# Performance work log

Measured on AMD Instinct MI355X. Metric: run time of the kernel, lower is better.

The kernel has to match this reference:

```python
import jax, jax.numpy as jnp
import numpy as np
from jax import lax

B, N, C = 4, 3072, 512
SAMPLE_RATIO = 0.25
CLUSTER_NUM = int(np.ceil(N * SAMPLE_RATIO))  # 768, static (mask=None, no 'r')
K = 5  # self.k, since k <= cluster_num


def setup_inputs() -> dict:
    key = jax.random.key(0)
    k1, = jax.random.split(key, 1)
    x = jax.random.normal(k1, (B, N, C), dtype=jnp.float32)
    # idx_token starts as identity mapping per batch (standard TCFormer init)
    idx_token = jnp.tile(jnp.arange(N, dtype=jnp.int32)[None, :], (B, 1))
    agg_weight = jnp.ones((B, N, 1), dtype=jnp.float32)
    return {"x": x, "idx_token": idx_token, "agg_weight": agg_weight}


def _cluster_dpc_knn(x):
    # runs under no_grad in torch -> stop_gradient here
    xs = lax.stop_gradient(x).astype(jnp.float32)
    sq = jnp.sum(xs * xs, axis=-1)  # [B,N]
    d2 = sq[:, :, None] + sq[:, None, :] - 2.0 * jnp.einsum('bnc,bmc->bnm', xs, xs)
    dist = jnp.sqrt(jnp.maximum(d2, 0.0)) / jnp.sqrt(jnp.float32(C))  # cdist / C**0.5
    # k nearest (smallest) distances
    neg_nearest, _ = lax.top_k(-dist, K)
    dist_nearest = -neg_nearest  # [B,N,K]
    density = jnp.exp(-jnp.mean(dist_nearest ** 2, axis=-1))
    density = density + jax.random.uniform(jax.random.key(42), density.shape, dtype=density.dtype) * 1e-6
    mask = (density[:, None, :] > density[:, :, None]).astype(x.dtype)  # [B,N,N]
    dist_max = jnp.max(dist.reshape(B, -1), axis=-1)[:, None, None]
    dist_min = jnp.min(dist * mask + dist_max * (1.0 - mask), axis=-1)  # [B,N]
    score = dist_min * density
    _, index_down = lax.top_k(score, CLUSTER_NUM)  # [B,cluster]
    # gather rows of dist at cluster centers, assign each token to nearest center
    dmat = jnp.take_along_axis(dist, index_down[:, :, None], axis=1)  # [B,cluster,N]
    idx_cluster = jnp.argmin(dmat, axis=1).astype(jnp.int32)  # [B,N]
    # force centers to map to their own cluster id
    idx_cluster = idx_cluster.at[jnp.arange(B)[:, None], index_down].set(
        jnp.broadcast_to(jnp.arange(CLUSTER_NUM, dtype=jnp.int32)[None, :], (B, CLUSTER_NUM)))
    return idx_cluster


def reference(x, idx_token, agg_weight):
    idx_cluster = _cluster_dpc_knn(x)
    # merge_tokens
    token_weight = jnp.ones((B, N, 1), dtype=x.dtype)
    idx = idx_cluster + jnp.arange(B, dtype=jnp.int32)[:, None] * CLUSTER_NUM  # [B,N]
    idx_flat = idx.reshape(-1)
    all_weight = jax.ops.segment_sum(token_weight.reshape(-1), idx_flat,
                                     num_segments=B * CLUSTER_NUM) + 1e-6  # [B*cluster]
    norm_weight = token_weight / all_weight[idx_flat].reshape(B, N, 1)  # [B,N,1]
    x_merged = jax.ops.segment_sum((x * norm_weight).reshape(B * N, C), idx_flat,
                                   num_segments=B * CLUSTER_NUM).reshape(B, CLUSTER_NUM, C)
    idx_token_new = jnp.take_along_axis(idx_cluster, idx_token, axis=1)  # [B,N]
    weight_t = jnp.take_along_axis(norm_weight, idx_token[:, :, None], axis=1)  # [B,N,1]
    agg_weight_new = agg_weight * weight_t
    return x_merged, agg_weight_new, idx_token_new, idx_cluster
```

## Files before the change

### kernel.cpp

```cpp
#include <hip/hip_runtime.h>
#include <math.h>
#include <float.h>

constexpr int B  = 4;
constexpr int N  = 3072;
constexpr int C  = 512;
constexpr int CL = 768;

typedef unsigned short u16;
typedef __attribute__((ext_vector_type(8))) short s16x8;
typedef __attribute__((ext_vector_type(4))) float f32x4;

__device__ __forceinline__ unsigned rotl32(unsigned v, int d) { return (v << d) | (v >> (32 - d)); }

__device__ inline void threefry2x32(unsigned k0, unsigned k1, unsigned c0, unsigned c1,
                                    unsigned& o0, unsigned& o1) {
  unsigned ks0 = k0, ks1 = k1, ks2 = 0x1BD11BDAu ^ k0 ^ k1;
  unsigned x0 = c0 + ks0, x1 = c1 + ks1;
#define TF_RND(r) { x0 += x1; x1 = rotl32(x1, (r)); x1 ^= x0; }
  TF_RND(13) TF_RND(15) TF_RND(26) TF_RND(6)  x0 += ks1; x1 += ks2 + 1u;
  TF_RND(17) TF_RND(29) TF_RND(16) TF_RND(24) x0 += ks2; x1 += ks0 + 2u;
  TF_RND(13) TF_RND(15) TF_RND(26) TF_RND(6)  x0 += ks0; x1 += ks1 + 3u;
  TF_RND(17) TF_RND(29) TF_RND(16) TF_RND(24) x0 += ks1; x1 += ks2 + 4u;
  TF_RND(13) TF_RND(15) TF_RND(26) TF_RND(6)  x0 += ks2; x1 += ks0 + 5u;
#undef TF_RND
  o0 = x0; o1 = x1;
}

__device__ inline float jax_uniform_bn(int f) {
  constexpr int HALF = (B * N) / 2;
  unsigned o0, o1, bits;
  if (f < HALF) { threefry2x32(0u, 42u, (unsigned)f, (unsigned)(f + HALF), o0, o1); bits = o0; }
  else          { threefry2x32(0u, 42u, (unsigned)(f - HALF), (unsigned)f, o0, o1); bits = o1; }
  return __uint_as_float((bits >> 9) | 0x3f800000u) - 1.0f;
}

__device__ __forceinline__ u16 bf16rn(float f) {
  unsigned u = __float_as_uint(f);
  unsigned r = u + 0x7FFFu + ((u >> 16) & 1u);
  return (u16)(r >> 16);
}
__device__ __forceinline__ float bf16tof(u16 h) {
  return __uint_as_float(((unsigned)h) << 16);
}

__global__ __launch_bounds__(64) void k_prep(const float* __restrict__ x, float* __restrict__ sq,
                                             u16* __restrict__ xhi, u16* __restrict__ xlo,
                                             int* __restrict__ counts,
                                             unsigned long long* __restrict__ packed,
                                             float* __restrict__ distmax) {
  int row = blockIdx.x;
  int lane = threadIdx.x;
  const float* xr = x + (size_t)row * C;
  u16* hr = xhi + (size_t)row * C;
  u16* lr = xlo + (size_t)row * C;
  float s = 0.f;
  for (int c = lane * 4; c < C; c += 256) {
    float4 v = *(const float4*)(xr + c);
    s += v.x * v.x + v.y * v.y + v.z * v.z + v.w * v.w;
    u16 h0 = bf16rn(v.x), h1 = bf16rn(v.y), h2 = bf16rn(v.z), h3 = bf16rn(v.w);
    u16 l0 = bf16rn(v.x - bf16tof(h0));
    u16 l1 = bf16rn(v.y - bf16tof(h1));
    u16 l2 = bf16rn(v.z - bf16tof(h2));
    u16 l3 = bf16rn(v.w - bf16tof(h3));
    uint2 hp, lp;
    hp.x = (unsigned)h0 | ((unsigned)h1 << 16); hp.y = (unsigned)h2 | ((unsigned)h3 << 16);
    lp.x = (unsigned)l0 | ((unsigned)l1 << 16); lp.y = (unsigned)l2 | ((unsigned)l3 << 16);
    *(uint2*)(hr + c) = hp;
    *(uint2*)(lr + c) = lp;
  }
  for (int o = 32; o > 0; o >>= 1) s += __shfl_down(s, o, 64);
  if (lane == 0) {
    sq[row] = s;
    packed[row] = ~0ull;
    if (row < B * CL) counts[row] = 0;
    if (row < B) distmax[row] = 0.f;
  }
}

__device__ __forceinline__ void ins5b(float t[5], float v) {
  float c = v;
  float n;
  n = fminf(t[0], c); c = fmaxf(t[0], c); t[0] = n;
  n = fminf(t[1], c); c = fmaxf(t[1], c); t[1] = n;
  n = fminf(t[2], c); c = fmaxf(t[2], c); t[2] = n;
  n = fminf(t[3], c); c = fmaxf(t[3], c); t[3] = n;
  t[4] = fminf(t[4], c);
}

constexpr int NT3 = N / 128;
constexpr int NTILE3 = NT3 * (NT3 + 1) / 2;

__global__ __launch_bounds__(256, 2) void k_distm(const u16* __restrict__ xhi, const u16* __restrict__ xlo,
                                                  const float* __restrict__ sq,
                                                  float* __restrict__ distbuf,
                                                  float* __restrict__ part5, int b0) {
  __shared__ __align__(16) char smem[65536];
  u16* smem_u16 = (u16*)smem;

  int bl = blockIdx.y, b = b0 + bl;

  int bx = blockIdx.x;
  constexpr int NX = 8, QX = NTILE3 / NX, RX = NTILE3 % NX;
  int xcd = bx % NX, sub = bx / NX;
  int idx = (xcd < RX ? xcd * (QX + 1) : RX * (QX + 1) + (xcd - RX) * QX) + sub;

  int ti = 0, rem = idx;
  while (rem >= NT3 - ti) { rem -= NT3 - ti; ++ti; }
  int tj = ti + rem;
  int i0 = ti * 128, j0 = tj * 128;
  bool do_mirror = (ti != tj);

  const float* sqb = sq + (size_t)b * N;
  float* dist = distbuf + (size_t)bl * N * N;

  int tid = threadIdx.x;
  int lane = tid & 63, w = tid >> 6;
  int wr = (w >> 1) * 64, wc = (w & 1) * 64;
  int l15 = lane & 15, l4 = lane >> 4;
  int csw = (lane >> 1) & 3;

  const u16* hil = (w & 1) ? xlo : xhi;
  int rbase0 = (w < 2) ? i0 : j0;
  const u16* gsrc = hil + ((size_t)b * N + rbase0 + (lane >> 2)) * C
                        + ((lane & 3) ^ ((lane >> 3) & 3)) * 8;

  f32x4 acc[4][4];
#pragma unroll
  for (int rt = 0; rt < 4; ++rt)
#pragma unroll
    for (int ct = 0; ct < 4; ++ct)
#pragma unroll
      for (int e = 0; e < 4; ++e) acc[rt][ct][e] = 0.f;

  {
    u16* lb = smem_u16 + w * 4096;
#pragma unroll
    for (int q = 0; q < 8; ++q)
      __builtin_amdgcn_global_load_lds(
          (const __attribute__((address_space(1))) void*)(gsrc + q * 16 * C),
          (__attribute__((address_space(3))) void*)(lb + q * 512), 16, 0, 0);
  }
  __syncthreads();

#define KSTEP(CUR, STG, KNXT, DO_STAGE)                                              \
  {                                                                                  \
    if (DO_STAGE) {                                                                  \
      u16* lb = smem_u16 + (STG) * 16384 + w * 4096;                                 \
      const u16* gs = gsrc + (KNXT);                                                 \
      _Pragma("unroll")                                                              \
      for (int q = 0; q < 8; ++q)                                                    \
        __builtin_amdgcn_global_load_lds(                                            \
            (const __attribute__((address_space(1))) void*)(gs + q * 16 * C),        \
            (__attribute__((address_space(3))) void*)(lb + q * 512), 16, 0, 0);      \
    }                                                                                \
    const u16* sb = smem_u16 + (CUR) * 16384;                                        \
    s16x8 ah[4], al[4];                                                              \
    _Pragma("unroll")                                                                \
    for (int rt = 0; rt < 4; ++rt) {                                                 \
      int ro = (wr + rt * 16 + l15) * 32 + (l4 ^ csw) * 8;                           \
      ah[rt] = *(const s16x8*)(sb + ro);                                             \
      al[rt] = *(const s16x8*)(sb + 4096 + ro);                                      \
    }                                                                                \
    _Pragma("unroll")                                                                \
    for (int ct = 0; ct < 4; ++ct) {                                                 \
      int co = (wc + ct * 16 + l15) * 32 + (l4 ^ csw) * 8;                           \
      s16x8 bh = *(const s16x8*)(sb + 8192 + co);                                    \
      s16x8 bl = *(const s16x8*)(sb + 12288 + co);                                   \
      _Pragma("unroll")                                                              \
      for (int rt = 0; rt < 4; ++rt) {                                               \
        acc[rt][ct] = __builtin_amdgcn_mfma_f32_16x16x32_bf16(ah[rt], bh, acc[rt][ct], 0, 0, 0); \
        acc[rt][ct] = __builtin_amdgcn_mfma_f32_16x16x32_bf16(ah[rt], bl, acc[rt][ct], 0, 0, 0); \
        acc[rt][ct] = __builtin_amdgcn_mfma_f32_16x16x32_bf16(al[rt], bh, acc[rt][ct], 0, 0, 0); \
      }                                                                              \
    }                                                                                \
    __syncthreads();                                                                 \
  }

  for (int ks = 0; ks < 16; ks += 2) {
    KSTEP(0, 1, (ks + 1) * 32, true)
    KSTEP(1, 0, (ks + 2) * 32, (ks + 2 < 16))
  }
#undef KSTEP

  const float SQC = 22.627416997969522f;
  float sqi[4][4], sqj[4];
#pragma unroll
  for (int rt = 0; rt < 4; ++rt)
#pragma unroll
    for (int r = 0; r < 4; ++r) sqi[rt][r] = sqb[i0 + wr + rt * 16 + l4 * 4 + r];
#pragma unroll
  for (int ct = 0; ct < 4; ++ct) sqj[ct] = sqb[j0 + wc + ct * 16 + l15];

#pragma unroll
  for (int rt = 0; rt < 4; ++rt)
#pragma unroll
    for (int ct = 0; ct < 4; ++ct)
#pragma unroll
      for (int r = 0; r < 4; ++r) {
        float d2 = fmaxf(sqi[rt][r] + sqj[ct] - 2.0f * acc[rt][ct][r], 0.0f);
        acc[rt][ct][r] = sqrtf(d2) / SQC;
      }

  constexpr int TSTR = 77;
  float* sT = (float*)smem + w * (32 * TSTR);

  float t5A[5] = {FLT_MAX, FLT_MAX, FLT_MAX, FLT_MAX, FLT_MAX};
  float mxA = 0.f;

#pragma unroll
  for (int p = 0; p < 2; ++p) {
#pragma unroll
    for (int cth = 0; cth < 2; ++cth) {
      int ct = p * 2 + cth;
      int cl = cth * 16 + l15;
#pragma unroll
      for (int rt = 0; rt < 4; ++rt)
#pragma unroll
        for (int r = 0; r < 4; ++r)
          sT[cl * TSTR + rt * 16 + l4 * 4 + r] = acc[rt][ct][r];
    }
    {
      int g4 = lane & 7, rbase = lane >> 3;
#pragma unroll
      for (int it = 0; it < 8; ++it) {
        int rl = it * 8 + rbase;
        float4 v = make_float4(sT[(4 * g4 + 0) * TSTR + rl],
                               sT[(4 * g4 + 1) * TSTR + rl],
                               sT[(4 * g4 + 2) * TSTR + rl],
                               sT[(4 * g4 + 3) * TSTR + rl]);
        *(float4*)(dist + (size_t)(i0 + wr + rl) * N + j0 + wc + p * 32 + 4 * g4) = v;
      }
    }
    if (do_mirror) {
      int cg = lane >> 4, rq = lane & 15;
#pragma unroll
      for (int cc = 0; cc < 8; ++cc) {
        int c = cc * 4 + cg;
        float4 v;
        v.x = sT[c * TSTR + rq * 4 + 0];
        v.y = sT[c * TSTR + rq * 4 + 1];
        v.z = sT[c * TSTR + rq * 4 + 2];
        v.w = sT[c * TSTR + rq * 4 + 3];
        *(float4*)(dist + (size_t)(j0 + wc + p * 32 + c) * N + i0 + wr + rq * 4) = v;
      }
    }
    for (int c = 0; c < 32; ++c) {
      float v = sT[c * TSTR + lane];
      mxA = fmaxf(mxA, v);
      ins5b(t5A, v);
    }
    if (do_mirror) {
      int cl = lane & 31, half = lane >> 5;
      float t5B[5] = {FLT_MAX, FLT_MAX, FLT_MAX, FLT_MAX, FLT_MAX};
      float mxB = 0.f;
      for (int k = 0; k < 32; ++k) {
        float v = sT[cl * TSTR + half * 32 + k];
        mxB = fmaxf(mxB, v);
        ins5b(t5B, v);
      }
      mxB = fmaxf(mxB, __shfl_xor(mxB, 32, 64));
      float o0 = __shfl_xor(t5B[0], 32, 64);
      float o1 = __shfl_xor(t5B[1], 32, 64);
      float o2 = __shfl_xor(t5B[2], 32, 64);
      float o3 = __shfl_xor(t5B[3], 32, 64);
      float o4 = __shfl_xor(t5B[4], 32, 64);
      ins5b(t5B, o0); ins5b(t5B, o1); ins5b(t5B, o2); ins5b(t5B, o3); ins5b(t5B, o4);
      if (half == 0) {
        int rowB = j0 + wc + p * 32 + cl;
        int slotB = ti * 2 + (wr >> 6);
        float* dst = part5 + (((size_t)bl * 48 + slotB) * 6) * N + rowB;
        dst[0] = t5B[0]; dst[(size_t)N] = t5B[1]; dst[2 * (size_t)N] = t5B[2];
        dst[3 * (size_t)N] = t5B[3]; dst[4 * (size_t)N] = t5B[4]; dst[5 * (size_t)N] = mxB;
      }
    }
  }
  {
    int rowA = i0 + wr + lane;
    int slotA = tj * 2 + (wc >> 6);
    float* dst = part5 + (((size_t)bl * 48 + slotA) * 6) * N + rowA;
    dst[0] = t5A[0]; dst[(size_t)N] = t5A[1]; dst[2 * (size_t)N] = t5A[2];
    dst[3 * (size_t)N] = t5A[3]; dst[4 * (size_t)N] = t5A[4]; dst[5 * (size_t)N] = mxA;
  }
}

__global__ __launch_bounds__(256) void k_dens(const float* __restrict__ part5,
                                              float* __restrict__ density,
                                              float* __restrict__ distmax, int b0) {
  int g = blockIdx.x * 256 + threadIdx.x;
  int bl = g / N, r = g % N;
  int b = b0 + bl;
  const float* base = part5 + (size_t)bl * 48 * 6 * N + r;
  float t5[5] = {FLT_MAX, FLT_MAX, FLT_MAX, FLT_MAX, FLT_MAX};
  float mx = 0.f;
  for (int s = 0; s < 48; ++s) {
    const float* sp = base + (size_t)s * 6 * N;
    ins5b(t5, sp[0]);
    ins5b(t5, sp[(size_t)N]);
    ins5b(t5, sp[2 * (size_t)N]);
    ins5b(t5, sp[3 * (size_t)N]);
    ins5b(t5, sp[4 * (size_t)N]);
    mx = fmaxf(mx, sp[5 * (size_t)N]);
  }
  float sum = t5[0] * t5[0] + t5[1] * t5[1] + t5[2] * t5[2] + t5[3] * t5[3] + t5[4] * t5[4];
  density[b * N + r] = expf(-(sum / 5.0f)) + jax_uniform_bn(b * N + r) * 1e-6f;
#pragma unroll
  for (int m = 1; m < 64; m <<= 1) mx = fmaxf(mx, __shfl_xor(mx, m, 64));
  if ((threadIdx.x & 63) == 0) atomicMax((int*)(distmax + b), __float_as_int(mx));
}

__global__ __launch_bounds__(256) void k_maskmin(const float* __restrict__ distbuf,
                                                 const float* __restrict__ density,
                                                 const float* __restrict__ distmax,
                                                 float* __restrict__ score, int b0) {
  __shared__ float sd[N];
  int tid = threadIdx.x;
  int wv = tid >> 6, lane = tid & 63;
  int i = blockIdx.x * 4 + wv;
  int bl = blockIdx.y, b = b0 + bl;
  const float* db = density + (size_t)b * N;
  for (int j = tid * 4; j < N; j += 1024) *(float4*)(sd + j) = *(const float4*)(db + j);
  __syncthreads();
  float di = sd[i];
  float dmax = distmax[b];
  const float* row = distbuf + ((size_t)bl * N + i) * N;
  float mn = dmax;
#pragma unroll
  for (int it = 0; it < N / 256; ++it) {
    int j = it * 256 + lane * 4;
    float4 v = *(const float4*)(row + j);
    float4 d = *(const float4*)(sd + j);
    mn = fminf(mn, (d.x > di) ? v.x : dmax);
    mn = fminf(mn, (d.y > di) ? v.y : dmax);
    mn = fminf(mn, (d.z > di) ? v.z : dmax);
    mn = fminf(mn, (d.w > di) ? v.w : dmax);
  }
#pragma unroll
  for (int m = 1; m < 64; m <<= 1) mn = fminf(mn, __shfl_xor(mn, m, 64));
  if (lane == 0) score[b * N + i] = mn * di;
}

__global__ __launch_bounds__(256) void k_rank(const float* __restrict__ score,
                                              int* __restrict__ index_down,
                                              int* __restrict__ rank, int b0) {
  __shared__ float ssc[N];
  int tid = threadIdx.x;
  int wv = tid >> 6, lane = tid & 63;
  int i = blockIdx.x * 4 + wv;
  int b = b0 + blockIdx.y;
  const float* sb = score + (size_t)b * N;
  for (int j = tid * 4; j < N; j += 1024) *(float4*)(ssc + j) = *(const float4*)(sb + j);
  __syncthreads();
  float si = ssc[i];
  int cnt = 0;
#pragma unroll
  for (int it = 0; it < N / 256; ++it) {
    int j = it * 256 + lane * 4;
    float4 v = *(const float4*)(ssc + j);
    cnt += (v.x > si) || (v.x == si && (j + 0) < i);
    cnt += (v.y > si) || (v.y == si && (j + 1) < i);
    cnt += (v.z > si) || (v.z == si && (j + 2) < i);
    cnt += (v.w > si) || (v.w == si && (j + 3) < i);
  }
#pragma unroll
  for (int m = 1; m < 64; m <<= 1) cnt += __shfl_xor(cnt, m, 64);
  if (lane == 0) {
    rank[b * N + i] = (cnt < CL) ? cnt : -1;
    if (cnt < CL) index_down[b * CL + cnt] = i;
  }
}

__global__ __launch_bounds__(256) void k_assign_part(const float* __restrict__ distbuf,
                                                     const int* __restrict__ index_down,
                                                     unsigned long long* __restrict__ packed, int b0) {
  constexpr int RCH = CL / 8;
  __shared__ int sid[RCH];
  int bl = blockIdx.z, b = b0 + bl;
  int r0 = blockIdx.y * RCH;
  int tid = threadIdx.x;
  for (int r = tid; r < RCH; r += 256) sid[r] = index_down[b * CL + r0 + r];
  __syncthreads();
  int j = blockIdx.x * 256 + tid;
  const float* base = distbuf + (size_t)bl * N * N;
  float best = FLT_MAX; int bestr = 0;
#pragma unroll 8
  for (int r = 0; r < RCH; ++r) {
    float d = base[(size_t)sid[r] * N + j];
    if (d < best) { best = d; bestr = r0 + r; }
  }
  unsigned long long key = ((unsigned long long)__float_as_uint(best) << 32) | (unsigned)bestr;
  atomicMin(&packed[b * N + j], key);
}

__global__ void k_assign_fin2(const unsigned long long* __restrict__ packed,
                              const int* __restrict__ rank,
                              int* __restrict__ idx_cluster, int* __restrict__ counts) {
  int g = blockIdx.x * 256 + threadIdx.x;
  int b = g / N;
  int r = rank[g];
  int cl = (r >= 0) ? r : (int)(unsigned)(packed[g] & 0xffffffffull);
  idx_cluster[g] = cl;
  atomicAdd(&counts[b * CL + cl], 1);
}

__global__ __launch_bounds__(1024) void k_scan(const int* __restrict__ counts,
                                               int* __restrict__ offsets, int* __restrict__ cursor) {
  constexpr int T = B * CL;
  __shared__ int sm[T];
  int tid = threadIdx.x;
  for (int p = tid; p < T; p += 1024) sm[p] = counts[p];
  __syncthreads();
  for (int off = 1; off < T; off <<= 1) {
    int v[3]; int n = 0;
    for (int p = tid; p < T; p += 1024) { v[n++] = (p >= off) ? sm[p - off] : 0; }
    __syncthreads();
    n = 0;
    for (int p = tid; p < T; p += 1024) { sm[p] += v[n++]; }
    __syncthreads();
  }
  for (int p = tid; p < T; p += 1024) {
    int e = sm[p] - counts[p];
    offsets[p] = e; cursor[p] = e;
  }
}

__global__ void k_fill(const int* __restrict__ idx_cluster, int* __restrict__ cursor,
                       int* __restrict__ members) {
  int g = blockIdx.x * 256 + threadIdx.x;
  int b = g / N, i = g % N;
  int seg = b * CL + idx_cluster[g];
  int pos = atomicAdd(&cursor[seg], 1);
  members[pos] = i;
}

__global__ __launch_bounds__(128) void k_gather(const float* __restrict__ x, const int* __restrict__ members,
                                                const int* __restrict__ offsets, const int* __restrict__ counts,
                                                float* __restrict__ out0) {
  int seg = blockIdx.x;
  int b = seg / CL;
  int cnt = counts[seg], off = offsets[seg];
  float nw = 1.0f / ((float)cnt + 1e-6f);
  int c = threadIdx.x * 4;
  const float* xb = x + (size_t)b * N * C;
  float4 acc = make_float4(0.f, 0.f, 0.f, 0.f);
  for (int m = 0; m < cnt; ++m) {
    int tok = members[off + m];
    float4 v = *(const float4*)(xb + (size_t)tok * C + c);
    acc.x += v.x * nw; acc.y += v.y * nw; acc.z += v.z * nw; acc.w += v.w * nw;
  }
  *(float4*)(out0 + (size_t)seg * C + c) = acc;
}

__global__ void k_final(const float* __restrict__ agg_weight, const int* __restrict__ idx_token,
                        const int* __restrict__ idx_cluster, const int* __restrict__ counts,
                        float* __restrict__ out1, float* __restrict__ out2, float* __restrict__ out3) {
  int g = blockIdx.x * 256 + threadIdx.x;
  int b = g / N;
  int it = idx_token[g];
  int clt = idx_cluster[b * N + it];
  float nwt = 1.0f / ((float)counts[b * CL + clt] + 1e-6f);
  out1[g] = agg_weight[g] * nwt;
  out2[g] = (float)clt;
  out3[g] = (float)idx_cluster[g];
}

extern "C" void kernel_launch(void* const* d_in, const int* in_sizes, int n_in,
                              void* d_out, int out_size, void* d_ws, size_t ws_size,
                              hipStream_t stream) {
  const float* x          = (const float*)d_in[0];
  const int*   idx_token  = (const int*)d_in[1];
  const float* agg_weight = (const float*)d_in[2];

  float* out0 = (float*)d_out;
  float* out1 = out0 + (size_t)B * CL * C;
  float* out2 = out1 + (size_t)B * N;
  float* out3 = out2 + (size_t)B * N;

  char* w = (char*)d_ws;
  auto carve = [&](size_t bytes) { char* p = w; w += (bytes + 255) & ~(size_t)255; return p; };
  float*    sq         = (float*)carve((size_t)B * N * 4);
  float*    density    = (float*)carve((size_t)B * N * 4);
  float*    score      = (float*)carve((size_t)B * N * 4);
  float*    distmax    = (float*)carve((size_t)B * 4);
  int*      index_down = (int*)carve((size_t)B * CL * 4);
  int*      rank       = (int*)carve((size_t)B * N * 4);
  int*      idx_clus   = (int*)carve((size_t)B * N * 4);
  int*      counts     = (int*)carve((size_t)B * CL * 4);
  int*      offsets    = (int*)carve((size_t)B * CL * 4);
  int*      cursor     = (int*)carve((size_t)B * CL * 4);
  int*      members    = (int*)carve((size_t)B * N * 4);
  unsigned long long* packed = (unsigned long long*)carve((size_t)B * N * 8);
  u16*      xhi        = (u16*)carve((size_t)B * N * C * 2);
  u16*      xlo        = (u16*)carve((size_t)B * N * C * 2);
  float*    part5      = (float*)carve((size_t)B * 48 * 6 * N * 4);
  size_t used = (size_t)(w - (char*)d_ws);
  size_t per  = (size_t)N * N * 4;
  int nb_max = (ws_size > used) ? (int)((ws_size - used) / per) : 0;
  if (nb_max < 1) nb_max = 1;
  if (nb_max > B) nb_max = B;
  float* distbuf = (float*)w;

  k_prep<<<B * N, 64, 0, stream>>>(x, sq, xhi, xlo, counts, packed, distmax);

  for (int b0 = 0; b0 < B; b0 += nb_max) {
    int nb = (B - b0 < nb_max) ? (B - b0) : nb_max;
    k_distm<<<dim3(NTILE3, nb), 256, 0, stream>>>(xhi, xlo, sq, distbuf, part5, b0);
    k_dens<<<(nb * N) / 256, 256, 0, stream>>>(part5, density, distmax, b0);
    k_maskmin<<<dim3(N / 4, nb), 256, 0, stream>>>(distbuf, density, distmax, score, b0);
    k_rank<<<dim3(N / 4, nb), 256, 0, stream>>>(score, index_down, rank, b0);
    k_assign_part<<<dim3(N / 256, 8, nb), 256, 0, stream>>>(distbuf, index_down, packed, b0);
  }

  k_assign_fin2<<<(B * N) / 256, 256, 0, stream>>>(packed, rank, idx_clus, counts);
  k_scan<<<1, 1024, 0, stream>>>(counts, offsets, cursor);
  k_fill<<<(B * N) / 256, 256, 0, stream>>>(idx_clus, cursor, members);
  k_gather<<<B * CL, 128, 0, stream>>>(x, members, offsets, counts, out0);
  k_final<<<(B * N) / 256, 256, 0, stream>>>(agg_weight, idx_token, idx_clus, counts, out1, out2, out3);
}
```

Baseline: 294.2 us.

## Overlap GEMM LDS staging with partial vmcnt waits; batch four rows per wave

In the distance GEMM, the full __syncthreads after each k-step is replaced by raw s_barrier plus s_waitcnt vmcnt(8). This lets the next stage's global-to-LDS loads stay in flight while the current tile is consumed. The maskmin and rank kernels now process four rows per wave instead of one. That cuts the grid by four and reuses each LDS density/score load across four rows. The hand-placed waitcnt and barriers depend on exact counting of outstanding loads, and any miscount would be a correctness risk.

Result: no change. 293.3 us (-0.3%).

```diff
diff --git a/kernel.cpp b/kernel.cpp
--- a/kernel.cpp
+++ b/kernel.cpp
@@ -141,7 +141,6 @@
           (const __attribute__((address_space(1))) void*)(gsrc + q * 16 * C),
           (__attribute__((address_space(3))) void*)(lb + q * 512), 16, 0, 0);
   }
-  __syncthreads();
 
 #define KSTEP(CUR, STG, KNXT, DO_STAGE)                                              \
   {                                                                                  \
@@ -153,7 +152,12 @@
         __builtin_amdgcn_global_load_lds(                                            \
             (const __attribute__((address_space(1))) void*)(gs + q * 16 * C),        \
             (__attribute__((address_space(3))) void*)(lb + q * 512), 16, 0, 0);      \
+      asm volatile("s_waitcnt vmcnt(8)" ::: "memory");                               \
+    } else {                                                                         \
+      asm volatile("s_waitcnt vmcnt(0)" ::: "memory");                               \
     }                                                                                \
+    __builtin_amdgcn_s_barrier();                                                    \
+    asm volatile("" ::: "memory");                                                   \
     const u16* sb = smem_u16 + (CUR) * 16384;                                        \
     s16x8 ah[4], al[4];                                                              \
     _Pragma("unroll")                                                                \
@@ -174,7 +178,9 @@
         acc[rt][ct] = __builtin_amdgcn_mfma_f32_16x16x32_bf16(al[rt], bh, acc[rt][ct], 0, 0, 0); \
       }                                                                              \
     }                                                                                \
-    __syncthreads();                                                                 \
+    asm volatile("" ::: "memory");                                                   \
+    __builtin_amdgcn_s_barrier();                                                    \
+    asm volatile("" ::: "memory");                                                   \
   }
 
   for (int ks = 0; ks < 16; ks += 2) {
@@ -316,28 +322,53 @@
   __shared__ float sd[N];
   int tid = threadIdx.x;
   int wv = tid >> 6, lane = tid & 63;
-  int i = blockIdx.x * 4 + wv;
   int bl = blockIdx.y, b = b0 + bl;
   const float* db = density + (size_t)b * N;
   for (int j = tid * 4; j < N; j += 1024) *(float4*)(sd + j) = *(const float4*)(db + j);
   __syncthreads();
-  float di = sd[i];
+  int i0r = blockIdx.x * 16 + wv * 4;
   float dmax = distmax[b];
-  const float* row = distbuf + ((size_t)bl * N + i) * N;
-  float mn = dmax;
-#pragma unroll
+  const float* row0 = distbuf + ((size_t)bl * N + i0r) * N;
+  float di0 = sd[i0r], di1 = sd[i0r + 1], di2 = sd[i0r + 2], di3 = sd[i0r + 3];
+  float mn0 = dmax, mn1 = dmax, mn2 = dmax, mn3 = dmax;
+#pragma unroll 2
   for (int it = 0; it < N / 256; ++it) {
     int j = it * 256 + lane * 4;
-    float4 v = *(const float4*)(row + j);
-    float4 d = *(const float4*)(sd + j);
-    mn = fminf(mn, (d.x > di) ? v.x : dmax);
-    mn = fminf(mn, (d.y > di) ? v.y : dmax);
-    mn = fminf(mn, (d.z > di) ? v.z : dmax);
-    mn = fminf(mn, (d.w > di) ? v.w : dmax);
-  }
-#pragma unroll
-  for (int m = 1; m < 64; m <<= 1) mn = fminf(mn, __shfl_xor(mn, m, 64));
-  if (lane == 0) score[b * N + i] = mn * di;
+    float4 d  = *(const float4*)(sd + j);
+    float4 v0 = *(const float4*)(row0 + j);
+    float4 v1 = *(const float4*)(row0 + (size_t)N + j);
+    float4 v2 = *(const float4*)(row0 + 2 * (size_t)N + j);
+    float4 v3 = *(const float4*)(row0 + 3 * (size_t)N + j);
+    mn0 = fminf(mn0, (d.x > di0) ? v0.x : dmax);
+    mn0 = fminf(mn0, (d.y > di0) ? v0.y : dmax);
+    mn0 = fminf(mn0, (d.z > di0) ? v0.z : dmax);
+    mn0 = fminf(mn0, (d.w > di0) ? v0.w : dmax);
+    mn1 = fminf(mn1, (d.x > di1) ? v1.x : dmax);
+    mn1 = fminf(mn1, (d.y > di1) ? v1.y : dmax);
+    mn1 = fminf(mn1, (d.z > di1) ? v1.z : dmax);
+    mn1 = fminf(mn1, (d.w > di1) ? v1.w : dmax);
+    mn2 = fminf(mn2, (d.x > di2) ? v2.x : dmax);
+    mn2 = fminf(mn2, (d.y > di2) ? v2.y : dmax);
+    mn2 = fminf(mn2, (d.z > di2) ? v2.z : dmax);
+    mn2 = fminf(mn2, (d.w > di2) ? v2.w : dmax);
+    mn3 = fminf(mn3, (d.x > di3) ? v3.x : dmax);
+    mn3 = fminf(mn3, (d.y > di3) ? v3.y : dmax);
+    mn3 = fminf(mn3, (d.z > di3) ? v3.z : dmax);
+    mn3 = fminf(mn3, (d.w > di3) ? v3.w : dmax);
+  }
+#pragma unroll
+  for (int m = 1; m < 64; m <<= 1) {
+    mn0 = fminf(mn0, __shfl_xor(mn0, m, 64));
+    mn1 = fminf(mn1, __shfl_xor(mn1, m, 64));
+    mn2 = fminf(mn2, __shfl_xor(mn2, m, 64));
+    mn3 = fminf(mn3, __shfl_xor(mn3, m, 64));
+  }
+  if (lane == 0) {
+    score[b * N + i0r]     = mn0 * di0;
+    score[b * N + i0r + 1] = mn1 * di1;
+    score[b * N + i0r + 2] = mn2 * di2;
+    score[b * N + i0r + 3] = mn3 * di3;
+  }
 }
 
 __global__ __launch_bounds__(256) void k_rank(const float* __restrict__ score,
@@ -346,27 +377,50 @@
   __shared__ float ssc[N];
   int tid = threadIdx.x;
   int wv = tid >> 6, lane = tid & 63;
-  int i = blockIdx.x * 4 + wv;
   int b = b0 + blockIdx.y;
   const float* sb = score + (size_t)b * N;
   for (int j = tid * 4; j < N; j += 1024) *(float4*)(ssc + j) = *(const float4*)(sb + j);
   __syncthreads();
-  float si = ssc[i];
-  int cnt = 0;
-#pragma unroll
+  int i0r = blockIdx.x * 16 + wv * 4;
+  float s0 = ssc[i0r], s1 = ssc[i0r + 1], s2 = ssc[i0r + 2], s3 = ssc[i0r + 3];
+  int c0 = 0, c1 = 0, c2 = 0, c3 = 0;
+#pragma unroll 2
   for (int it = 0; it < N / 256; ++it) {
     int j = it * 256 + lane * 4;
     float4 v = *(const float4*)(ssc + j);
-    cnt += (v.x > si) || (v.x == si && (j + 0) < i);
-    cnt += (v.y > si) || (v.y == si && (j + 1) < i);
-    cnt += (v.z > si) || (v.z == si && (j + 2) < i);
-    cnt += (v.w > si) || (v.w == si && (j + 3) < i);
-  }
-#pragma unroll
-  for (int m = 1; m < 64; m <<= 1) cnt += __shfl_xor(cnt, m, 64);
+    c0 += (v.x > s0) || (v.x == s0 && (j + 0) < i0r);
+    c0 += (v.y > s0) || (v.y == s0 && (j + 1) < i0r);
+    c0 += (v.z > s0) || (v.z == s0 && (j + 2) < i0r);
+    c0 += (v.w > s0) || (v.w == s0 && (j + 3) < i0r);
+    c1 += (v.x > s1) || (v.x == s1 && (j + 0) < i0r + 1);
+    c1 += (v.y > s1) || (v.y == s1 && (j + 1) < i0r + 1);
+    c1 += (v.z > s1) || (v.z == s1 && (j + 2) < i0r + 1);
+    c1 += (v.w > s1) || (v.w == s1 && (j + 3) < i0r + 1);
+    c2 += (v.x > s2) || (v.x == s2 && (j + 0) < i0r + 2);
+    c2 += (v.y > s2) || (v.y == s2 && (j + 1) < i0r + 2);
+    c2 += (v.z > s2) || (v.z == s2 && (j + 2) < i0r + 2);
+    c2 += (v.w > s2) || (v.w == s2 && (j + 3) < i0r + 2);
+    c3 += (v.x > s3) || (v.x == s3 && (j + 0) < i0r + 3);
+    c3 += (v.y > s3) || (v.y == s3 && (j + 1) < i0r + 3);
+    c3 += (v.z > s3) || (v.z == s3 && (j + 2) < i0r + 3);
+    c3 += (v.w > s3) || (v.w == s3 && (j + 3) < i0r + 3);
+  }
+#pragma unroll
+  for (int m = 1; m < 64; m <<= 1) {
+    c0 += __shfl_xor(c0, m, 64);
+    c1 += __shfl_xor(c1, m, 64);
+    c2 += __shfl_xor(c2, m, 64);
+    c3 += __shfl_xor(c3, m, 64);
+  }
   if (lane == 0) {
-    rank[b * N + i] = (cnt < CL) ? cnt : -1;
-    if (cnt < CL) index_down[b * CL + cnt] = i;
+    rank[b * N + i0r]     = (c0 < CL) ? c0 : -1;
+    rank[b * N + i0r + 1] = (c1 < CL) ? c1 : -1;
+    rank[b * N + i0r + 2] = (c2 < CL) ? c2 : -1;
+    rank[b * N + i0r + 3] = (c3 < CL) ? c3 : -1;
+    if (c0 < CL) index_down[b * CL + c0] = i0r;
+    if (c1 < CL) index_down[b * CL + c1] = i0r + 1;
+    if (c2 < CL) index_down[b * CL + c2] = i0r + 2;
+    if (c3 < CL) index_down[b * CL + c3] = i0r + 3;
   }
 }
 
@@ -506,8 +560,8 @@
     int nb = (B - b0 < nb_max) ? (B - b0) : nb_max;
     k_distm<<<dim3(NTILE3, nb), 256, 0, stream>>>(xhi, xlo, sq, distbuf, part5, b0);
     k_dens<<<(nb * N) / 256, 256, 0, stream>>>(part5, density, distmax, b0);
-    k_maskmin<<<dim3(N / 4, nb), 256, 0, stream>>>(distbuf, density, distmax, score, b0);
-    k_rank<<<dim3(N / 4, nb), 256, 0, stream>>>(score, index_down, rank, b0);
+    k_maskmin<<<dim3(N / 16, nb), 256, 0, stream>>>(distbuf, density, distmax, score, b0);
+    k_rank<<<dim3(N / 16, nb), 256, 0, stream>>>(score, index_down, rank, b0);
     k_assign_part<<<dim3(N / 256, 8, nb), 256, 0, stream>>>(distbuf, index_down, packed, b0);
   }
 
```
